# Optimization experiments

Measured on AMD Instinct MI355X. Metric: run time of the kernel, lower is better.

Reference implementation:

```python
import jax, jax.numpy as jnp
import numpy as np

HEADS = 4
DIM_HEAD = 32
DIM = 128
EPS = 1e-5


def layer_norm(x, g, b):
    m = jnp.mean(x, axis=-1, keepdims=True)
    v = jnp.var(x, axis=-1, keepdims=True)
    return (x - m) * jax.lax.rsqrt(v + EPS) * g + b


def setup_inputs() -> dict:
    key = jax.random.key(0)
    ks = jax.random.split(key, 24)
    B, D, Hb, Wb = 1, DIM, 50, 50
    N, h, w = 6, 24, 44
    Q = Hb * Wb
    NK = N * h * w
    inner = HEADS * DIM_HEAD
    s = 0.02
    inp = {
        'q': jax.random.normal(ks[0], (B, D, Hb, Wb), jnp.float32),
        'k': jax.random.normal(ks[1], (B, N, D, h, w), jnp.float32),
        'v': jax.random.normal(ks[2], (B, N, D, h, w), jnp.float32),
        'W_logits': jax.random.uniform(ks[3], (B, Q, NK), jnp.float32),
        'vis': jax.random.randint(ks[4], (B, Q, NK), 0, 2, jnp.int32),
        'skip': jax.random.normal(ks[5], (B, D, Hb, Wb), jnp.float32),
        'qn_g': jnp.ones((D,)), 'qn_b': jnp.zeros((D,)),
        'kn_g': jnp.ones((D,)), 'kn_b': jnp.zeros((D,)),
        'vn_g': jnp.ones((D,)), 'vn_b': jnp.zeros((D,)),
        'wq': s * jax.random.normal(ks[6], (inner, D)), 'bq': jnp.zeros((inner,)),
        'wk': s * jax.random.normal(ks[7], (inner, D)), 'bk': jnp.zeros((inner,)),
        'wv': s * jax.random.normal(ks[8], (inner, D)), 'bv': jnp.zeros((inner,)),
        'wproj': s * jax.random.normal(ks[9], (D, inner)), 'bproj': jnp.zeros((D,)),
        'pre_g': jnp.ones((D,)), 'pre_b': jnp.zeros((D,)),
        'w1': s * jax.random.normal(ks[10], (2 * D, D)), 'b1': jnp.zeros((2 * D,)),
        'w2': s * jax.random.normal(ks[11], (D, 2 * D)), 'b2': jnp.zeros((D,)),
        'post_g': jnp.ones((D,)), 'post_b': jnp.zeros((D,)),
    }
    return inp


def reference(q, k, v, W_logits, vis, skip,
              qn_g, qn_b, kn_g, kn_b, vn_g, vn_b,
              wq, bq, wk, bk, wv, bv, wproj, bproj,
              pre_g, pre_b, w1, b1, w2, b2, post_g, post_b):
    B, D, Hb, Wb = q.shape
    Q = Hb * Wb
    scale = DIM_HEAD ** (-0.5)
    # flatten: q -> [B, Q, D]; k,v [B,N,D,h,w] -> [B, NK, D]
    qf = q.reshape(B, D, Q).transpose(0, 2, 1)
    kf = jnp.transpose(k, (0, 1, 3, 4, 2)).reshape(B, -1, D)
    vf = jnp.transpose(v, (0, 1, 3, 4, 2)).reshape(B, -1, D)
    qf = layer_norm(qf, qn_g, qn_b) @ wq.T + bq
    kf = layer_norm(kf, kn_g, kn_b) @ wk.T + bk
    vf = layer_norm(vf, vn_g, vn_b) @ wv.T + bv
    # split heads -> [B, H, Q/K, dh]
    qh = qf.reshape(B, Q, HEADS, DIM_HEAD).transpose(0, 2, 1, 3)
    kh = kf.reshape(B, -1, HEADS, DIM_HEAD).transpose(0, 2, 1, 3)
    vh = vf.reshape(B, -1, HEADS, DIM_HEAD).transpose(0, 2, 1, 3)
    logits = jnp.einsum('bhqd,bhkd->bhqk', qh, kh) * scale
    neg_inf = jnp.finfo(logits.dtype).min
    logits = jnp.where(vis[:, None] == 0, neg_inf, logits)
    logits = logits * W_logits[:, None]
    attn = jax.nn.softmax(logits, axis=-1)
    out = jnp.einsum('bhqk,bhkd->bhqd', attn, vh)
    out = out.transpose(0, 2, 1, 3).reshape(B, Q, HEADS * DIM_HEAD)
    out = out @ wproj.T + bproj
    z = out.transpose(0, 2, 1).reshape(B, D, Hb, Wb) + skip
    zf = z.reshape(B, D, Q).transpose(0, 2, 1)
    zf = layer_norm(zf, pre_g, pre_b)
    hmid = jax.nn.gelu(zf @ w1.T + b1, approximate=False)
    zf = zf + (hmid @ w2.T + b2)
    zf = layer_norm(zf, post_g, post_b)
    return zf.transpose(0, 2, 1).reshape(B, D, Hb, Wb)
```

## Files before the change

### kernel.cpp

```cpp
#include <hip/hip_runtime.h>
#include <hip/hip_bf16.h>

typedef __attribute__((ext_vector_type(8))) short bf16x8;
typedef __attribute__((ext_vector_type(4))) float f32x4;

#define NQ 2500
#define NKK 6336
#define NHEADS 4
#define DHEAD 32
#define CSC 0.25503482f
#define BIGNEG (-1.0e30f)

#define WS_QP 0
#define WS_KP 640000
#define WS_VT 2262016
#define WS_WB 3884032
#define WS_OP 4146176
#define OSPLIT_F 340000
#define OROW_F 136
#define WS_REQ3 8226176ULL

#define WQB 0
#define WKB 16384
#define WVB 32768
#define WPROJB 49152
#define W1B 65536
#define W2B 98304

#define NTILES_TOTAL 99
#define TQ 16
#define ATQ 32
#define TK 64
#define QBLOCKS 157
#define AQBLOCKS 79

#define PSTR 72
#define ABSTR 68

__device__ __forceinline__ unsigned short bf16bits(float x) {
  union { __hip_bfloat16 h; unsigned short s; } cv;
  cv.h = __float2bfloat16(x);
  return cv.s;
}

__global__ __launch_bounds__(256) void wconv_kernel(
    const float* __restrict__ wq, const float* __restrict__ wk,
    const float* __restrict__ wv, const float* __restrict__ wproj,
    const float* __restrict__ w1, const float* __restrict__ w2,
    __hip_bfloat16* __restrict__ wb)
{
  int e = (blockIdx.x * 256 + threadIdx.x) * 4;
  const float* src; int off;
  if (e < 16384)      { src = wq;    off = e; }
  else if (e < 32768) { src = wk;    off = e - 16384; }
  else if (e < 49152) { src = wv;    off = e - 32768; }
  else if (e < 65536) { src = wproj; off = e - 49152; }
  else if (e < 98304) { src = w1;    off = e - 65536; }
  else                { src = w2;    off = e - 98304; }
  float4 v = *(const float4*)(src + off);
  ushort4 o4;
  o4.x = bf16bits(v.x); o4.y = bf16bits(v.y); o4.z = bf16bits(v.z); o4.w = bf16bits(v.w);
  *(ushort4*)((unsigned short*)wb + e) = o4;
}

__global__ __launch_bounds__(256) void lnproj_kernel(
    const float* __restrict__ qin, const float* __restrict__ kin, const float* __restrict__ vin,
    const float* __restrict__ qn_g, const float* __restrict__ qn_b,
    const float* __restrict__ kn_g, const float* __restrict__ kn_b,
    const float* __restrict__ vn_g, const float* __restrict__ vn_b,
    const __hip_bfloat16* __restrict__ wball,
    const float* __restrict__ bq, const float* __restrict__ bk, const float* __restrict__ bv,
    __hip_bfloat16* __restrict__ Qp, __hip_bfloat16* __restrict__ Kp,
    __hip_bfloat16* __restrict__ Vt)
{
  __shared__ __hip_bfloat16 lxb[32][136];
  __shared__ float lpart[32][8][2];
  __shared__ float lmr[32][2];
  __shared__ float lgb[128], lbeb[128];

  const int t = threadIdx.x;
  const int bb = blockIdx.x;
  int mode, row0;
  const float *in, *g, *be, *bo;
  const __hip_bfloat16* wb;
  if (bb < 79)       { mode = 0; row0 = bb * 32;         in = qin; g = qn_g; be = qn_b; wb = wball + WQB; bo = bq; }
  else if (bb < 277) { mode = 1; row0 = (bb - 79) * 32;  in = kin; g = kn_g; be = kn_b; wb = wball + WKB; bo = bk; }
  else               { mode = 2; row0 = (bb - 277) * 32; in = vin; g = vn_g; be = vn_b; wb = wball + WVB; bo = bv; }

  if (t < 128) { lgb[t] = g[t]; lbeb[t] = be[t]; }

  const int row = t & 31, seg = t >> 5;
  int grow = row0 + row;
  size_t base, dstr;
  bool rvalid = true;
  if (mode == 0) { rvalid = (grow < NQ); base = (size_t)(rvalid ? grow : NQ - 1); dstr = NQ; }
  else { int n = grow / 1056, rr = grow - n * 1056; base = (size_t)n * 135168 + rr; dstr = 1056; }

  float xr[16];
  float s = 0.f, ss = 0.f;
  #pragma unroll
  for (int i = 0; i < 16; ++i) {
    float x = in[base + (size_t)(seg * 16 + i) * dstr];
    xr[i] = x; s += x; ss += x * x;
  }
  lpart[row][seg][0] = s; lpart[row][seg][1] = ss;
  __syncthreads();
  if (t < 32) {
    float S = 0.f, SS = 0.f;
    #pragma unroll
    for (int j = 0; j < 8; ++j) { S += lpart[t][j][0]; SS += lpart[t][j][1]; }
    float mean = S * (1.f / 128.f);
    float var  = SS * (1.f / 128.f) - mean * mean;
    lmr[t][0] = mean;
    lmr[t][1] = rsqrtf(fmaxf(var, 0.f) + 1e-5f);
  }
  __syncthreads();
  {
    float mean = lmr[row][0], rstd = lmr[row][1];
    #pragma unroll
    for (int i = 0; i < 16; ++i) {
      int d = seg * 16 + i;
      lxb[row][d] = __float2bfloat16((xr[i] - mean) * rstd * lgb[d] + lbeb[d]);
    }
  }
  __syncthreads();

  const int wid = t >> 6, lane = t & 63;
  const int n16 = lane & 15, quad = lane >> 4;
  const int ow = wid * 32;

  f32x4 acc[2][2] = {};
  for (int kt = 0; kt < 4; ++kt) {
    bf16x8 af[2];
    #pragma unroll
    for (int mi = 0; mi < 2; ++mi)
      af[mi] = *(const bf16x8*)&lxb[mi * 16 + n16][kt * 32 + quad * 8];
    #pragma unroll
    for (int ni = 0; ni < 2; ++ni) {
      bf16x8 bw = *(const bf16x8*)(wb + (size_t)(ow + ni * 16 + n16) * 128 + kt * 32 + quad * 8);
      #pragma unroll
      for (int mi = 0; mi < 2; ++mi)
        acc[mi][ni] = __builtin_amdgcn_mfma_f32_16x16x32_bf16(af[mi], bw, acc[mi][ni], 0, 0, 0);
    }
  }

  float bias[2];
  #pragma unroll
  for (int ni = 0; ni < 2; ++ni) bias[ni] = bo[ow + ni * 16 + n16];

  #pragma unroll
  for (int mi = 0; mi < 2; ++mi) {
    int gr0 = row0 + mi * 16 + quad * 4;
    if (mode == 2) {
      #pragma unroll
      for (int ni = 0; ni < 2; ++ni) {
        int o = ow + ni * 16 + n16;
        ushort4 v4;
        v4.x = bf16bits(acc[mi][ni][0] + bias[ni]);
        v4.y = bf16bits(acc[mi][ni][1] + bias[ni]);
        v4.z = bf16bits(acc[mi][ni][2] + bias[ni]);
        v4.w = bf16bits(acc[mi][ni][3] + bias[ni]);
        *(ushort4*)((unsigned short*)Vt + (size_t)o * NKK + gr0) = v4;
      }
    } else {
      #pragma unroll
      for (int rg = 0; rg < 4; ++rg) {
        int gr = gr0 + rg;
        if (mode != 0 || gr < NQ) {
          #pragma unroll
          for (int ni = 0; ni < 2; ++ni) {
            int o = ow + ni * 16 + n16;
            __hip_bfloat16 b16 = __float2bfloat16(acc[mi][ni][rg] + bias[ni]);
            if (mode == 0) Qp[(size_t)gr * 128 + o] = b16;
            else           Kp[(size_t)gr * 128 + o] = b16;
          }
        }
      }
    }
  }
}

__global__ __launch_bounds__(256, 4) void attn_kernel(
    const __hip_bfloat16* __restrict__ Qp,
    const __hip_bfloat16* __restrict__ Kp,
    const __hip_bfloat16* __restrict__ Vt,
    const float* __restrict__ Wl,
    const int* __restrict__ vis,
    float* __restrict__ Opart)
{
  __shared__ alignas(16) float sc[2][ATQ * ABSTR];
  __shared__ alignas(16) __hip_bfloat16 lp[NHEADS * ATQ * PSTR];

  const int t = threadIdx.x;
  const int lane = t & 63;
  const int h = t >> 6;
  const int n16 = lane & 15;
  const int quad = lane >> 4;
  const int q0 = blockIdx.x * ATQ;
  const int split = blockIdx.y;
  const int ksplit = gridDim.y;
  const int tstart = (NTILES_TOTAL * split) / ksplit;
  const int ntiles = (NTILES_TOTAL * (split + 1)) / ksplit - tstart;

  bf16x8 aq[2];
  #pragma unroll
  for (int m = 0; m < 2; ++m) {
    int gqa = q0 + m * 16 + n16; if (gqa >= NQ) gqa = NQ - 1;
    aq[m] = *(const bf16x8*)(Qp + (size_t)gqa * 128 + h * DHEAD + quad * 8);
  }

  const int qq = t >> 3, kkc = (t & 7) * 8;
  int gqe = q0 + qq; if (gqe >= NQ) gqe = NQ - 1;
  const size_t wbase = (size_t)gqe * NKK + kkc;

  bf16x8 bones;
  {
    short one = (short)0x3F80;
    short val = (n16 == 0) ? one : (short)0;
    #pragma unroll
    for (int j = 0; j < 8; ++j) bones[j] = val;
  }

  float4 pw0, pw1; int4 pvs0, pvs1;

  auto issue = [&](int tile) {
    int k0 = (tstart + tile) * TK;
    pw0  = *(const float4*)(Wl + wbase + k0);
    pw1  = *(const float4*)(Wl + wbase + k0 + 4);
    pvs0 = *(const int4*)(vis + wbase + k0);
    pvs1 = *(const int4*)(vis + wbase + k0 + 4);
  };
  auto commit = [&](int buf) {
    float4 c0, c1;
    c0.x = pvs0.x ? pw0.x * CSC : BIGNEG * pw0.x;
    c0.y = pvs0.y ? pw0.y * CSC : BIGNEG * pw0.y;
    c0.z = pvs0.z ? pw0.z * CSC : BIGNEG * pw0.z;
    c0.w = pvs0.w ? pw0.w * CSC : BIGNEG * pw0.w;
    c1.x = pvs1.x ? pw1.x * CSC : BIGNEG * pw1.x;
    c1.y = pvs1.y ? pw1.y * CSC : BIGNEG * pw1.y;
    c1.z = pvs1.z ? pw1.z * CSC : BIGNEG * pw1.z;
    c1.w = pvs1.w ? pw1.w * CSC : BIGNEG * pw1.w;
    *(float4*)&sc[buf][qq * ABSTR + kkc] = c0;
    *(float4*)&sc[buf][qq * ABSTR + kkc + 4] = c1;
  };

  f32x4 o[2][3];
  #pragma unroll
  for (int m = 0; m < 2; ++m)
    #pragma unroll
    for (int j = 0; j < 3; ++j)
      o[m][j] = f32x4{0.f, 0.f, 0.f, 0.f};

  issue(0);
  commit(0);
  __syncthreads();

  for (int kt = 0; kt < ntiles; ++kt) {
    const int k0 = (tstart + kt) * TK;
    const int cur = kt & 1;
    if (kt + 1 < ntiles) issue(kt + 1);

    f32x4 s[2][4];
    #pragma unroll
    for (int ks = 0; ks < 4; ++ks) {
      bf16x8 bk = *(const bf16x8*)(Kp + (size_t)(k0 + ks * 16 + n16) * 128 + h * DHEAD + quad * 8);
      f32x4 z = {0.f, 0.f, 0.f, 0.f};
      s[0][ks] = __builtin_amdgcn_mfma_f32_16x16x32_bf16(aq[0], bk, z, 0, 0, 0);
      s[1][ks] = __builtin_amdgcn_mfma_f32_16x16x32_bf16(aq[1], bk, z, 0, 0, 0);
    }

    bf16x8 bv[2][2];
    #pragma unroll
    for (int kk = 0; kk < 2; ++kk) {
      bv[kk][0] = *(const bf16x8*)(Vt + (size_t)(h * DHEAD + n16) * NKK + k0 + kk * 32 + quad * 8);
      bv[kk][1] = *(const bf16x8*)(Vt + (size_t)(h * DHEAD + 16 + n16) * NKK + k0 + kk * 32 + quad * 8);
    }

    #pragma unroll
    for (int m = 0; m < 2; ++m) {
      #pragma unroll
      for (int ks = 0; ks < 4; ++ks) {
        #pragma unroll
        for (int r = 0; r < 4; ++r) {
          int row = m * 16 + quad * 4 + r;
          float c = sc[cur][row * ABSTR + ks * 16 + n16];
          float tt = s[m][ks][r] * c;
          float arg = (c >= 0.f) ? tt : c;
          float p = exp2f(fminf(arg, 60.f));
          lp[h * (ATQ * PSTR) + row * PSTR + ks * 16 + n16] = __float2bfloat16(p);
        }
      }
    }

    #pragma unroll
    for (int kk = 0; kk < 2; ++kk) {
      #pragma unroll
      for (int m = 0; m < 2; ++m) {
        bf16x8 ap = *(const bf16x8*)&lp[h * (ATQ * PSTR) + (m * 16 + n16) * PSTR + kk * 32 + quad * 8];
        o[m][0] = __builtin_amdgcn_mfma_f32_16x16x32_bf16(ap, bv[kk][0], o[m][0], 0, 0, 0);
        o[m][1] = __builtin_amdgcn_mfma_f32_16x16x32_bf16(ap, bv[kk][1], o[m][1], 0, 0, 0);
        o[m][2] = __builtin_amdgcn_mfma_f32_16x16x32_bf16(ap, bones, o[m][2], 0, 0, 0);
      }
    }

    if (kt + 1 < ntiles) {
      commit(cur ^ 1);
      __syncthreads();
    }
  }

  #pragma unroll
  for (int m = 0; m < 2; ++m) {
    #pragma unroll
    for (int r = 0; r < 4; ++r) {
      int gq = q0 + m * 16 + quad * 4 + r;
      if (gq < NQ) {
        float* rowp = Opart + (size_t)split * OSPLIT_F + (size_t)gq * OROW_F;
        rowp[h * DHEAD + n16] = o[m][0][r];
        rowp[h * DHEAD + 16 + n16] = o[m][1][r];
        if (n16 == 0) rowp[128 + h] = o[m][2][r];
      }
    }
  }
}

__global__ __launch_bounds__(256) void mlp_kernel(
    const float* __restrict__ Opart, int ksplit,
    const float* __restrict__ skip,
    const __hip_bfloat16* __restrict__ wball,
    const float* __restrict__ bproj,
    const float* __restrict__ pre_g, const float* __restrict__ pre_b,
    const float* __restrict__ b1, const float* __restrict__ b2,
    const float* __restrict__ post_g, const float* __restrict__ post_b,
    float* __restrict__ out)
{
  __shared__ __hip_bfloat16 sab[16][136];
  __shared__ __hip_bfloat16 znb[16][136];
  __shared__ float znf[16][132];
  __shared__ __hip_bfloat16 hb[16][264];
  __shared__ float part[16][4][2];

  const __hip_bfloat16* wprojb = wball + WPROJB;
  const __hip_bfloat16* w1b    = wball + W1B;
  const __hip_bfloat16* w2b    = wball + W2B;

  const int t = threadIdx.x;
  const int q0 = blockIdx.x * TQ;

  {
    int row = t >> 4, c0 = (t & 15) * 8;
    int gq = q0 + row; int cq = gq < NQ ? gq : NQ - 1;
    int head = c0 >> 5;
    float ll = 0.f;
    float acc8[8] = {};
    for (int s = 0; s < ksplit; ++s) {
      const float* rp = Opart + (size_t)s * OSPLIT_F + (size_t)cq * OROW_F;
      ll += rp[128 + head];
      float4 a = *(const float4*)(rp + c0);
      float4 b = *(const float4*)(rp + c0 + 4);
      acc8[0] += a.x; acc8[1] += a.y; acc8[2] += a.z; acc8[3] += a.w;
      acc8[4] += b.x; acc8[5] += b.y; acc8[6] += b.z; acc8[7] += b.w;
    }
    float rll = 1.f / fmaxf(ll, 1e-30f);
    #pragma unroll
    for (int i = 0; i < 8; ++i)
      sab[row][c0 + i] = __float2bfloat16(acc8[i] * rll);
  }
  __syncthreads();

  const int wid = t >> 6, lane = t & 63;
  const int n16 = lane & 15, quad = lane >> 4;
  const int qrow0 = q0 + quad * 4;

  f32x4 acc1[2] = {};
  for (int kt = 0; kt < 4; ++kt) {
    bf16x8 af = *(const bf16x8*)&sab[n16][kt * 32 + quad * 8];
    #pragma unroll
    for (int ni = 0; ni < 2; ++ni) {
      int o = wid * 32 + ni * 16 + n16;
      bf16x8 bw = *(const bf16x8*)(wprojb + (size_t)o * 128 + kt * 32 + quad * 8);
      acc1[ni] = __builtin_amdgcn_mfma_f32_16x16x32_bf16(af, bw, acc1[ni], 0, 0, 0);
    }
  }
  float z[2][4];
  #pragma unroll
  for (int ni = 0; ni < 2; ++ni) {
    int o = wid * 32 + ni * 16 + n16;
    float bo = bproj[o];
    if (qrow0 + 3 < NQ) {
      float4 sk = *(const float4*)(skip + (size_t)o * NQ + qrow0);
      z[ni][0] = acc1[ni][0] + bo + sk.x;
      z[ni][1] = acc1[ni][1] + bo + sk.y;
      z[ni][2] = acc1[ni][2] + bo + sk.z;
      z[ni][3] = acc1[ni][3] + bo + sk.w;
    } else {
      #pragma unroll
      for (int rg = 0; rg < 4; ++rg) {
        int cq = qrow0 + rg < NQ ? qrow0 + rg : NQ - 1;
        z[ni][rg] = acc1[ni][rg] + bo + skip[(size_t)o * NQ + cq];
      }
    }
  }
  #pragma unroll
  for (int rg = 0; rg < 4; ++rg) {
    float s = z[0][rg] + z[1][rg];
    float ss = z[0][rg] * z[0][rg] + z[1][rg] * z[1][rg];
    s += __shfl_xor(s, 1);  ss += __shfl_xor(ss, 1);
    s += __shfl_xor(s, 2);  ss += __shfl_xor(ss, 2);
    s += __shfl_xor(s, 4);  ss += __shfl_xor(ss, 4);
    s += __shfl_xor(s, 8);  ss += __shfl_xor(ss, 8);
    if (n16 == 0) { part[quad * 4 + rg][wid][0] = s; part[quad * 4 + rg][wid][1] = ss; }
  }
  __syncthreads();
  #pragma unroll
  for (int rg = 0; rg < 4; ++rg) {
    int row = quad * 4 + rg;
    float S  = part[row][0][0] + part[row][1][0] + part[row][2][0] + part[row][3][0];
    float SS = part[row][0][1] + part[row][1][1] + part[row][2][1] + part[row][3][1];
    float mean = S * (1.f / 128.f);
    float var  = SS * (1.f / 128.f) - mean * mean;
    float rstd = rsqrtf(fmaxf(var, 0.f) + 1e-5f);
    #pragma unroll
    for (int ni = 0; ni < 2; ++ni) {
      int o = wid * 32 + ni * 16 + n16;
      float zn = (z[ni][rg] - mean) * rstd * pre_g[o] + pre_b[o];
      znf[row][o] = zn;
      znb[row][o] = __float2bfloat16(zn);
    }
  }
  __syncthreads();

  f32x4 acc2[4] = {};
  for (int kt = 0; kt < 4; ++kt) {
    bf16x8 af = *(const bf16x8*)&znb[n16][kt * 32 + quad * 8];
    #pragma unroll
    for (int ni = 0; ni < 4; ++ni) {
      int j = wid * 64 + ni * 16 + n16;
      bf16x8 bw = *(const bf16x8*)(w1b + (size_t)j * 128 + kt * 32 + quad * 8);
      acc2[ni] = __builtin_amdgcn_mfma_f32_16x16x32_bf16(af, bw, acc2[ni], 0, 0, 0);
    }
  }
  #pragma unroll
  for (int ni = 0; ni < 4; ++ni) {
    int j = wid * 64 + ni * 16 + n16;
    float bj = b1[j];
    #pragma unroll
    for (int rg = 0; rg < 4; ++rg) {
      float a1 = acc2[ni][rg] + bj;
      hb[quad * 4 + rg][j] = __float2bfloat16(0.5f * a1 * (1.0f + erff(a1 * 0.70710678118654752f)));
    }
  }
  __syncthreads();

  f32x4 acc3[2] = {};
  for (int kt = 0; kt < 8; ++kt) {
    bf16x8 af = *(const bf16x8*)&hb[n16][kt * 32 + quad * 8];
    #pragma unroll
    for (int ni = 0; ni < 2; ++ni) {
      int o = wid * 32 + ni * 16 + n16;
      bf16x8 bw = *(const bf16x8*)(w2b + (size_t)o * 256 + kt * 32 + quad * 8);
      acc3[ni] = __builtin_amdgcn_mfma_f32_16x16x32_bf16(af, bw, acc3[ni], 0, 0, 0);
    }
  }
  float y[2][4];
  #pragma unroll
  for (int ni = 0; ni < 2; ++ni) {
    int o = wid * 32 + ni * 16 + n16;
    float bo = b2[o];
    #pragma unroll
    for (int rg = 0; rg < 4; ++rg)
      y[ni][rg] = znf[quad * 4 + rg][o] + acc3[ni][rg] + bo;
  }
  #pragma unroll
  for (int rg = 0; rg < 4; ++rg) {
    float s = y[0][rg] + y[1][rg];
    float ss = y[0][rg] * y[0][rg] + y[1][rg] * y[1][rg];
    s += __shfl_xor(s, 1);  ss += __shfl_xor(ss, 1);
    s += __shfl_xor(s, 2);  ss += __shfl_xor(ss, 2);
    s += __shfl_xor(s, 4);  ss += __shfl_xor(ss, 4);
    s += __shfl_xor(s, 8);  ss += __shfl_xor(ss, 8);
    if (n16 == 0) { part[quad * 4 + rg][wid][0] = s; part[quad * 4 + rg][wid][1] = ss; }
  }
  __syncthreads();
  #pragma unroll
  for (int rg = 0; rg < 4; ++rg) {
    int row = quad * 4 + rg;
    float S  = part[row][0][0] + part[row][1][0] + part[row][2][0] + part[row][3][0];
    float SS = part[row][0][1] + part[row][1][1] + part[row][2][1] + part[row][3][1];
    float mean = S * (1.f / 128.f);
    float var  = SS * (1.f / 128.f) - mean * mean;
    float rstd = rsqrtf(fmaxf(var, 0.f) + 1e-5f);
    #pragma unroll
    for (int ni = 0; ni < 2; ++ni) {
      int o = wid * 32 + ni * 16 + n16;
      y[ni][rg] = (y[ni][rg] - mean) * rstd * post_g[o] + post_b[o];
    }
  }
  #pragma unroll
  for (int ni = 0; ni < 2; ++ni) {
    int o = wid * 32 + ni * 16 + n16;
    if (qrow0 + 3 < NQ) {
      *(float4*)(out + (size_t)o * NQ + qrow0) = make_float4(y[ni][0], y[ni][1], y[ni][2], y[ni][3]);
    } else {
      #pragma unroll
      for (int rg = 0; rg < 4; ++rg)
        if (qrow0 + rg < NQ) out[(size_t)o * NQ + qrow0 + rg] = y[ni][rg];
    }
  }
}

extern "C" void kernel_launch(void* const* d_in, const int* in_sizes, int n_in,
                              void* d_out, int out_size, void* d_ws, size_t ws_size,
                              hipStream_t stream) {
  if (ws_size < WS_REQ3) return;
  int ksplit = (int)((ws_size - WS_OP) / (size_t)(OSPLIT_F * 4));
  if (ksplit > 12) ksplit = 12;
  if (ksplit < 3)  ksplit = 3;

  const float* q     = (const float*)d_in[0];
  const float* k     = (const float*)d_in[1];
  const float* v     = (const float*)d_in[2];
  const float* Wl    = (const float*)d_in[3];
  const int*   vis   = (const int*)d_in[4];
  const float* skip  = (const float*)d_in[5];
  const float* qn_g  = (const float*)d_in[6];
  const float* qn_b  = (const float*)d_in[7];
  const float* kn_g  = (const float*)d_in[8];
  const float* kn_b  = (const float*)d_in[9];
  const float* vn_g  = (const float*)d_in[10];
  const float* vn_b  = (const float*)d_in[11];
  const float* wq    = (const float*)d_in[12];
  const float* bq    = (const float*)d_in[13];
  const float* wk    = (const float*)d_in[14];
  const float* bk    = (const float*)d_in[15];
  const float* wv    = (const float*)d_in[16];
  const float* bv    = (const float*)d_in[17];
  const float* wproj = (const float*)d_in[18];
  const float* bproj = (const float*)d_in[19];
  const float* pre_g = (const float*)d_in[20];
  const float* pre_b = (const float*)d_in[21];
  const float* w1    = (const float*)d_in[22];
  const float* b1    = (const float*)d_in[23];
  const float* w2    = (const float*)d_in[24];
  const float* b2    = (const float*)d_in[25];
  const float* post_g= (const float*)d_in[26];
  const float* post_b= (const float*)d_in[27];

  char* ws = (char*)d_ws;
  __hip_bfloat16* Qp = (__hip_bfloat16*)(ws + WS_QP);
  __hip_bfloat16* Kp = (__hip_bfloat16*)(ws + WS_KP);
  __hip_bfloat16* Vt = (__hip_bfloat16*)(ws + WS_VT);
  __hip_bfloat16* Wb = (__hip_bfloat16*)(ws + WS_WB);
  float* Opart = (float*)(ws + WS_OP);

  hipLaunchKernelGGL(wconv_kernel, dim3(128), dim3(256), 0, stream,
                     wq, wk, wv, wproj, w1, w2, Wb);

  hipLaunchKernelGGL(lnproj_kernel, dim3(475), dim3(256), 0, stream,
                     q, k, v, qn_g, qn_b, kn_g, kn_b, vn_g, vn_b,
                     Wb, bq, bk, bv, Qp, Kp, Vt);

  hipLaunchKernelGGL(attn_kernel, dim3(AQBLOCKS, ksplit), dim3(256), 0, stream,
                     Qp, Kp, Vt, Wl, vis, Opart);

  hipLaunchKernelGGL(mlp_kernel, dim3(QBLOCKS), dim3(256), 0, stream,
                     Opart, ksplit, skip, Wb, bproj, pre_g, pre_b,
                     b1, b2, post_g, post_b, (float*)d_out);
}
```

Measured before the change: 248.1 us.

## Use nontemporal loads/stores in attention, flatten grid with split-major ordering, cap ksplit

The W_logits and vis streams, which are read once, now go through nontemporal loads, and the partial-output stores are nontemporal too, to reduce cache pollution. The 2D grid becomes a 1D grid in which the k-splits of one query block are adjacent, so neighbouring blocks share the same Q rows. The maximum ksplit drops from 12 to 8, which cuts the partial-sum work in the MLP kernel but gives fewer blocks to fill the GPU.

New measurement: 266.4 us. 1.07x slower.

```diff
diff --git a/kernel.cpp b/kernel.cpp
--- a/kernel.cpp
+++ b/kernel.cpp
@@ -3,6 +3,8 @@
 
 typedef __attribute__((ext_vector_type(8))) short bf16x8;
 typedef __attribute__((ext_vector_type(4))) float f32x4;
+typedef __attribute__((ext_vector_type(4))) float f4v;
+typedef __attribute__((ext_vector_type(4))) int i4v;
 
 #define NQ 2500
 #define NKK 6336
@@ -196,9 +198,10 @@
   const int h = t >> 6;
   const int n16 = lane & 15;
   const int quad = lane >> 4;
-  const int q0 = blockIdx.x * ATQ;
-  const int split = blockIdx.y;
-  const int ksplit = gridDim.y;
+  const int ksplit = gridDim.x / AQBLOCKS;
+  const int split = blockIdx.x % ksplit;
+  const int qb = blockIdx.x / ksplit;
+  const int q0 = qb * ATQ;
   const int tstart = (NTILES_TOTAL * split) / ksplit;
   const int ntiles = (NTILES_TOTAL * (split + 1)) / ksplit - tstart;
 
@@ -221,27 +224,27 @@
     for (int j = 0; j < 8; ++j) bones[j] = val;
   }
 
-  float4 pw0, pw1; int4 pvs0, pvs1;
+  f4v pw0, pw1; i4v pvs0, pvs1;
 
   auto issue = [&](int tile) {
     int k0 = (tstart + tile) * TK;
-    pw0  = *(const float4*)(Wl + wbase + k0);
-    pw1  = *(const float4*)(Wl + wbase + k0 + 4);
-    pvs0 = *(const int4*)(vis + wbase + k0);
-    pvs1 = *(const int4*)(vis + wbase + k0 + 4);
+    pw0  = __builtin_nontemporal_load((const f4v*)(Wl + wbase + k0));
+    pw1  = __builtin_nontemporal_load((const f4v*)(Wl + wbase + k0 + 4));
+    pvs0 = __builtin_nontemporal_load((const i4v*)(vis + wbase + k0));
+    pvs1 = __builtin_nontemporal_load((const i4v*)(vis + wbase + k0 + 4));
   };
   auto commit = [&](int buf) {
-    float4 c0, c1;
-    c0.x = pvs0.x ? pw0.x * CSC : BIGNEG * pw0.x;
-    c0.y = pvs0.y ? pw0.y * CSC : BIGNEG * pw0.y;
-    c0.z = pvs0.z ? pw0.z * CSC : BIGNEG * pw0.z;
-    c0.w = pvs0.w ? pw0.w * CSC : BIGNEG * pw0.w;
-    c1.x = pvs1.x ? pw1.x * CSC : BIGNEG * pw1.x;
-    c1.y = pvs1.y ? pw1.y * CSC : BIGNEG * pw1.y;
-    c1.z = pvs1.z ? pw1.z * CSC : BIGNEG * pw1.z;
-    c1.w = pvs1.w ? pw1.w * CSC : BIGNEG * pw1.w;
-    *(float4*)&sc[buf][qq * ABSTR + kkc] = c0;
-    *(float4*)&sc[buf][qq * ABSTR + kkc + 4] = c1;
+    f4v c0, c1;
+    c0[0] = pvs0[0] ? pw0[0] * CSC : BIGNEG * pw0[0];
+    c0[1] = pvs0[1] ? pw0[1] * CSC : BIGNEG * pw0[1];
+    c0[2] = pvs0[2] ? pw0[2] * CSC : BIGNEG * pw0[2];
+    c0[3] = pvs0[3] ? pw0[3] * CSC : BIGNEG * pw0[3];
+    c1[0] = pvs1[0] ? pw1[0] * CSC : BIGNEG * pw1[0];
+    c1[1] = pvs1[1] ? pw1[1] * CSC : BIGNEG * pw1[1];
+    c1[2] = pvs1[2] ? pw1[2] * CSC : BIGNEG * pw1[2];
+    c1[3] = pvs1[3] ? pw1[3] * CSC : BIGNEG * pw1[3];
+    *(f4v*)&sc[buf][qq * ABSTR + kkc] = c0;
+    *(f4v*)&sc[buf][qq * ABSTR + kkc + 4] = c1;
   };
 
   f32x4 o[2][3];
@@ -316,9 +319,9 @@
       int gq = q0 + m * 16 + quad * 4 + r;
       if (gq < NQ) {
         float* rowp = Opart + (size_t)split * OSPLIT_F + (size_t)gq * OROW_F;
-        rowp[h * DHEAD + n16] = o[m][0][r];
-        rowp[h * DHEAD + 16 + n16] = o[m][1][r];
-        if (n16 == 0) rowp[128 + h] = o[m][2][r];
+        __builtin_nontemporal_store(o[m][0][r], &rowp[h * DHEAD + n16]);
+        __builtin_nontemporal_store(o[m][1][r], &rowp[h * DHEAD + 16 + n16]);
+        if (n16 == 0) __builtin_nontemporal_store(o[m][2][r], &rowp[128 + h]);
       }
     }
   }
@@ -514,8 +517,8 @@
                               hipStream_t stream) {
   if (ws_size < WS_REQ3) return;
   int ksplit = (int)((ws_size - WS_OP) / (size_t)(OSPLIT_F * 4));
-  if (ksplit > 12) ksplit = 12;
-  if (ksplit < 3)  ksplit = 3;
+  if (ksplit > 8) ksplit = 8;
+  if (ksplit < 3) ksplit = 3;
 
   const float* q     = (const float*)d_in[0];
   const float* k     = (const float*)d_in[1];
@@ -560,7 +563,7 @@
                      q, k, v, qn_g, qn_b, kn_g, kn_b, vn_g, vn_b,
                      Wb, bq, bk, bv, Qp, Kp, Vt);
 
-  hipLaunchKernelGGL(attn_kernel, dim3(AQBLOCKS, ksplit), dim3(256), 0, stream,
+  hipLaunchKernelGGL(attn_kernel, dim3(AQBLOCKS * ksplit), dim3(256), 0, stream,
                      Qp, Kp, Vt, Wl, vis, Opart);
 
   hipLaunchKernelGGL(mlp_kernel, dim3(QBLOCKS), dim3(256), 0, stream,
```

## Halve attention query tile to 16 rows with XOR-swizzled LDS and more k-splits

Applied to the files above, without the earlier changes.

The attention kernel's query tile shrinks from 32 to 16 rows, so each wave runs a single MFMA row block. The padded LDS strides are replaced by XOR-swizzled layouts for the score-coefficient and probability buffers, and the occupancy hint rises from 4 to 5 blocks per CU. The k-split cap rises from 12 to 16 to create more parallel blocks. The trade-off is that each K/V tile loaded from global memory is now reused across half as many queries, so K/V traffic roughly doubles.

Result: slower. 291.4 us (+17.4%).

```diff
diff --git a/kernel.cpp b/kernel.cpp
--- a/kernel.cpp
+++ b/kernel.cpp
@@ -3,6 +3,8 @@
 
 typedef __attribute__((ext_vector_type(8))) short bf16x8;
 typedef __attribute__((ext_vector_type(4))) float f32x4;
+typedef __attribute__((ext_vector_type(4))) float f4v;
+typedef __attribute__((ext_vector_type(4))) int i4v;
 
 #define NQ 2500
 #define NKK 6336
@@ -29,13 +31,10 @@
 
 #define NTILES_TOTAL 99
 #define TQ 16
-#define ATQ 32
+#define ATQ 16
 #define TK 64
 #define QBLOCKS 157
-#define AQBLOCKS 79
-
-#define PSTR 72
-#define ABSTR 68
+#define AQBLOCKS 157
 
 __device__ __forceinline__ unsigned short bf16bits(float x) {
   union { __hip_bfloat16 h; unsigned short s; } cv;
@@ -180,7 +179,7 @@
   }
 }
 
-__global__ __launch_bounds__(256, 4) void attn_kernel(
+__global__ __launch_bounds__(256, 5) void attn_kernel(
     const __hip_bfloat16* __restrict__ Qp,
     const __hip_bfloat16* __restrict__ Kp,
     const __hip_bfloat16* __restrict__ Vt,
@@ -188,8 +187,8 @@
     const int* __restrict__ vis,
     float* __restrict__ Opart)
 {
-  __shared__ alignas(16) float sc[2][ATQ * ABSTR];
-  __shared__ alignas(16) __hip_bfloat16 lp[NHEADS * ATQ * PSTR];
+  __shared__ alignas(16) float sc[2][ATQ * 64];
+  __shared__ alignas(16) __hip_bfloat16 lp[NHEADS][ATQ * 64];
 
   const int t = threadIdx.x;
   const int lane = t & 63;
@@ -202,16 +201,16 @@
   const int tstart = (NTILES_TOTAL * split) / ksplit;
   const int ntiles = (NTILES_TOTAL * (split + 1)) / ksplit - tstart;
 
-  bf16x8 aq[2];
-  #pragma unroll
-  for (int m = 0; m < 2; ++m) {
-    int gqa = q0 + m * 16 + n16; if (gqa >= NQ) gqa = NQ - 1;
-    aq[m] = *(const bf16x8*)(Qp + (size_t)gqa * 128 + h * DHEAD + quad * 8);
-  }
-
-  const int qq = t >> 3, kkc = (t & 7) * 8;
+  bf16x8 aq;
+  {
+    int gqa = q0 + n16; if (gqa >= NQ) gqa = NQ - 1;
+    aq = *(const bf16x8*)(Qp + (size_t)gqa * 128 + h * DHEAD + quad * 8);
+  }
+
+  const int qq = t >> 4, kkc = (t & 15) * 4;
   int gqe = q0 + qq; if (gqe >= NQ) gqe = NQ - 1;
   const size_t wbase = (size_t)gqe * NKK + kkc;
+  const int scw = qq * 64 + (kkc ^ ((qq & 7) << 2));
 
   bf16x8 bones;
   {
@@ -221,35 +220,23 @@
     for (int j = 0; j < 8; ++j) bones[j] = val;
   }
 
-  float4 pw0, pw1; int4 pvs0, pvs1;
+  f4v pw; i4v pvs;
 
   auto issue = [&](int tile) {
     int k0 = (tstart + tile) * TK;
-    pw0  = *(const float4*)(Wl + wbase + k0);
-    pw1  = *(const float4*)(Wl + wbase + k0 + 4);
-    pvs0 = *(const int4*)(vis + wbase + k0);
-    pvs1 = *(const int4*)(vis + wbase + k0 + 4);
+    pw  = *(const f4v*)(Wl + wbase + k0);
+    pvs = *(const i4v*)(vis + wbase + k0);
   };
   auto commit = [&](int buf) {
-    float4 c0, c1;
-    c0.x = pvs0.x ? pw0.x * CSC : BIGNEG * pw0.x;
-    c0.y = pvs0.y ? pw0.y * CSC : BIGNEG * pw0.y;
-    c0.z = pvs0.z ? pw0.z * CSC : BIGNEG * pw0.z;
-    c0.w = pvs0.w ? pw0.w * CSC : BIGNEG * pw0.w;
-    c1.x = pvs1.x ? pw1.x * CSC : BIGNEG * pw1.x;
-    c1.y = pvs1.y ? pw1.y * CSC : BIGNEG * pw1.y;
-    c1.z = pvs1.z ? pw1.z * CSC : BIGNEG * pw1.z;
-    c1.w = pvs1.w ? pw1.w * CSC : BIGNEG * pw1.w;
-    *(float4*)&sc[buf][qq * ABSTR + kkc] = c0;
-    *(float4*)&sc[buf][qq * ABSTR + kkc + 4] = c1;
+    f4v c;
+    c[0] = pvs[0] ? pw[0] * CSC : BIGNEG * pw[0];
+    c[1] = pvs[1] ? pw[1] * CSC : BIGNEG * pw[1];
+    c[2] = pvs[2] ? pw[2] * CSC : BIGNEG * pw[2];
+    c[3] = pvs[3] ? pw[3] * CSC : BIGNEG * pw[3];
+    *(f4v*)&sc[buf][scw] = c;
   };
 
-  f32x4 o[2][3];
-  #pragma unroll
-  for (int m = 0; m < 2; ++m)
-    #pragma unroll
-    for (int j = 0; j < 3; ++j)
-      o[m][j] = f32x4{0.f, 0.f, 0.f, 0.f};
+  f32x4 o0 = {0.f,0.f,0.f,0.f}, o1 = {0.f,0.f,0.f,0.f}, o2 = {0.f,0.f,0.f,0.f};
 
   issue(0);
   commit(0);
@@ -260,13 +247,12 @@
     const int cur = kt & 1;
     if (kt + 1 < ntiles) issue(kt + 1);
 
-    f32x4 s[2][4];
+    f32x4 s[4];
     #pragma unroll
     for (int ks = 0; ks < 4; ++ks) {
       bf16x8 bk = *(const bf16x8*)(Kp + (size_t)(k0 + ks * 16 + n16) * 128 + h * DHEAD + quad * 8);
       f32x4 z = {0.f, 0.f, 0.f, 0.f};
-      s[0][ks] = __builtin_amdgcn_mfma_f32_16x16x32_bf16(aq[0], bk, z, 0, 0, 0);
-      s[1][ks] = __builtin_amdgcn_mfma_f32_16x16x32_bf16(aq[1], bk, z, 0, 0, 0);
+      s[ks] = __builtin_amdgcn_mfma_f32_16x16x32_bf16(aq, bk, z, 0, 0, 0);
     }
 
     bf16x8 bv[2][2];
@@ -277,30 +263,24 @@
     }
 
     #pragma unroll
-    for (int m = 0; m < 2; ++m) {
+    for (int ks = 0; ks < 4; ++ks) {
       #pragma unroll
-      for (int ks = 0; ks < 4; ++ks) {
-        #pragma unroll
-        for (int r = 0; r < 4; ++r) {
-          int row = m * 16 + quad * 4 + r;
-          float c = sc[cur][row * ABSTR + ks * 16 + n16];
-          float tt = s[m][ks][r] * c;
-          float arg = (c >= 0.f) ? tt : c;
-          float p = exp2f(fminf(arg, 60.f));
-          lp[h * (ATQ * PSTR) + row * PSTR + ks * 16 + n16] = __float2bfloat16(p);
-        }
+      for (int r = 0; r < 4; ++r) {
+        int row = quad * 4 + r;
+        float c = sc[cur][row * 64 + ((ks * 16 + n16) ^ ((row & 7) << 2))];
+        float tt = s[ks][r] * c;
+        float arg = (c >= 0.f) ? tt : c;
+        float p = exp2f(fminf(arg, 60.f));
+        lp[h][row * 64 + ((ks * 16 + n16) ^ ((row & 7) << 3))] = __float2bfloat16(p);
       }
     }
 
     #pragma unroll
     for (int kk = 0; kk < 2; ++kk) {
-      #pragma unroll
-      for (int m = 0; m < 2; ++m) {
-        bf16x8 ap = *(const bf16x8*)&lp[h * (ATQ * PSTR) + (m * 16 + n16) * PSTR + kk * 32 + quad * 8];
-        o[m][0] = __builtin_amdgcn_mfma_f32_16x16x32_bf16(ap, bv[kk][0], o[m][0], 0, 0, 0);
-        o[m][1] = __builtin_amdgcn_mfma_f32_16x16x32_bf16(ap, bv[kk][1], o[m][1], 0, 0, 0);
-        o[m][2] = __builtin_amdgcn_mfma_f32_16x16x32_bf16(ap, bones, o[m][2], 0, 0, 0);
-      }
+      bf16x8 ap = *(const bf16x8*)&lp[h][n16 * 64 + ((kk * 32 + quad * 8) ^ ((n16 & 7) << 3))];
+      o0 = __builtin_amdgcn_mfma_f32_16x16x32_bf16(ap, bv[kk][0], o0, 0, 0, 0);
+      o1 = __builtin_amdgcn_mfma_f32_16x16x32_bf16(ap, bv[kk][1], o1, 0, 0, 0);
+      o2 = __builtin_amdgcn_mfma_f32_16x16x32_bf16(ap, bones, o2, 0, 0, 0);
     }
 
     if (kt + 1 < ntiles) {
@@ -310,16 +290,13 @@
   }
 
   #pragma unroll
-  for (int m = 0; m < 2; ++m) {
-    #pragma unroll
-    for (int r = 0; r < 4; ++r) {
-      int gq = q0 + m * 16 + quad * 4 + r;
-      if (gq < NQ) {
-        float* rowp = Opart + (size_t)split * OSPLIT_F + (size_t)gq * OROW_F;
-        rowp[h * DHEAD + n16] = o[m][0][r];
-        rowp[h * DHEAD + 16 + n16] = o[m][1][r];
-        if (n16 == 0) rowp[128 + h] = o[m][2][r];
-      }
+  for (int r = 0; r < 4; ++r) {
+    int gq = q0 + quad * 4 + r;
+    if (gq < NQ) {
+      float* rowp = Opart + (size_t)split * OSPLIT_F + (size_t)gq * OROW_F;
+      rowp[h * DHEAD + n16] = o0[r];
+      rowp[h * DHEAD + 16 + n16] = o1[r];
+      if (n16 == 0) rowp[128 + h] = o2[r];
     }
   }
 }
@@ -514,7 +491,7 @@
                               hipStream_t stream) {
   if (ws_size < WS_REQ3) return;
   int ksplit = (int)((ws_size - WS_OP) / (size_t)(OSPLIT_F * 4));
-  if (ksplit > 12) ksplit = 12;
+  if (ksplit > 16) ksplit = 16;
   if (ksplit < 3)  ksplit = 3;
 
   const float* q     = (const float*)d_in[0];
```

## Double attention query tile to 64 with 512-thread blocks sharing K/V tiles

Applied to the files above, without the earlier changes.

The attention kernel now processes 64 queries per block using 8 waves (4 heads x 2 query halves), so each K/V tile fetched from global memory serves twice as many queries and the block count halves. The scale/mask tile shrinks to a single shared-memory buffer, with an extra barrier before refilling it in place of double buffering. The per-wave probability buffer is kept. The trade-off is an extra synchronisation per tile and lower occupancy (launch bounds 512,2), in exchange for fewer redundant K/V loads.

New measurement: 250.3 us. Within noise of the previous version (+0.9%).

```diff
diff --git a/kernel.cpp b/kernel.cpp
--- a/kernel.cpp
+++ b/kernel.cpp
@@ -29,10 +29,10 @@
 
 #define NTILES_TOTAL 99
 #define TQ 16
-#define ATQ 32
+#define ATQ 64
 #define TK 64
 #define QBLOCKS 157
-#define AQBLOCKS 79
+#define AQBLOCKS 40
 
 #define PSTR 72
 #define ABSTR 68
@@ -180,7 +180,7 @@
   }
 }
 
-__global__ __launch_bounds__(256, 4) void attn_kernel(
+__global__ __launch_bounds__(512, 2) void attn_kernel(
     const __hip_bfloat16* __restrict__ Qp,
     const __hip_bfloat16* __restrict__ Kp,
     const __hip_bfloat16* __restrict__ Vt,
@@ -188,12 +188,14 @@
     const int* __restrict__ vis,
     float* __restrict__ Opart)
 {
-  __shared__ alignas(16) float sc[2][ATQ * ABSTR];
-  __shared__ alignas(16) __hip_bfloat16 lp[NHEADS * ATQ * PSTR];
+  __shared__ alignas(16) float sc[ATQ * ABSTR];
+  __shared__ alignas(16) __hip_bfloat16 lp[8][32 * PSTR];
 
   const int t = threadIdx.x;
   const int lane = t & 63;
-  const int h = t >> 6;
+  const int w = t >> 6;
+  const int h = w & 3;
+  const int qh = w >> 2;
   const int n16 = lane & 15;
   const int quad = lane >> 4;
   const int q0 = blockIdx.x * ATQ;
@@ -205,7 +207,7 @@
   bf16x8 aq[2];
   #pragma unroll
   for (int m = 0; m < 2; ++m) {
-    int gqa = q0 + m * 16 + n16; if (gqa >= NQ) gqa = NQ - 1;
+    int gqa = q0 + qh * 32 + m * 16 + n16; if (gqa >= NQ) gqa = NQ - 1;
     aq[m] = *(const bf16x8*)(Qp + (size_t)gqa * 128 + h * DHEAD + quad * 8);
   }
 
@@ -230,7 +232,7 @@
     pvs0 = *(const int4*)(vis + wbase + k0);
     pvs1 = *(const int4*)(vis + wbase + k0 + 4);
   };
-  auto commit = [&](int buf) {
+  auto commit = [&]() {
     float4 c0, c1;
     c0.x = pvs0.x ? pw0.x * CSC : BIGNEG * pw0.x;
     c0.y = pvs0.y ? pw0.y * CSC : BIGNEG * pw0.y;
@@ -240,8 +242,8 @@
     c1.y = pvs1.y ? pw1.y * CSC : BIGNEG * pw1.y;
     c1.z = pvs1.z ? pw1.z * CSC : BIGNEG * pw1.z;
     c1.w = pvs1.w ? pw1.w * CSC : BIGNEG * pw1.w;
-    *(float4*)&sc[buf][qq * ABSTR + kkc] = c0;
-    *(float4*)&sc[buf][qq * ABSTR + kkc + 4] = c1;
+    *(float4*)&sc[qq * ABSTR + kkc] = c0;
+    *(float4*)&sc[qq * ABSTR + kkc + 4] = c1;
   };
 
   f32x4 o[2][3];
@@ -252,12 +254,11 @@
       o[m][j] = f32x4{0.f, 0.f, 0.f, 0.f};
 
   issue(0);
-  commit(0);
+  commit();
   __syncthreads();
 
   for (int kt = 0; kt < ntiles; ++kt) {
     const int k0 = (tstart + kt) * TK;
-    const int cur = kt & 1;
     if (kt + 1 < ntiles) issue(kt + 1);
 
     f32x4 s[2][4];
@@ -283,11 +284,11 @@
         #pragma unroll
         for (int r = 0; r < 4; ++r) {
           int row = m * 16 + quad * 4 + r;
-          float c = sc[cur][row * ABSTR + ks * 16 + n16];
+          float c = sc[(qh * 32 + row) * ABSTR + ks * 16 + n16];
           float tt = s[m][ks][r] * c;
           float arg = (c >= 0.f) ? tt : c;
           float p = exp2f(fminf(arg, 60.f));
-          lp[h * (ATQ * PSTR) + row * PSTR + ks * 16 + n16] = __float2bfloat16(p);
+          lp[w][row * PSTR + ks * 16 + n16] = __float2bfloat16(p);
         }
       }
     }
@@ -296,7 +297,7 @@
     for (int kk = 0; kk < 2; ++kk) {
       #pragma unroll
       for (int m = 0; m < 2; ++m) {
-        bf16x8 ap = *(const bf16x8*)&lp[h * (ATQ * PSTR) + (m * 16 + n16) * PSTR + kk * 32 + quad * 8];
+        bf16x8 ap = *(const bf16x8*)&lp[w][(m * 16 + n16) * PSTR + kk * 32 + quad * 8];
         o[m][0] = __builtin_amdgcn_mfma_f32_16x16x32_bf16(ap, bv[kk][0], o[m][0], 0, 0, 0);
         o[m][1] = __builtin_amdgcn_mfma_f32_16x16x32_bf16(ap, bv[kk][1], o[m][1], 0, 0, 0);
         o[m][2] = __builtin_amdgcn_mfma_f32_16x16x32_bf16(ap, bones, o[m][2], 0, 0, 0);
@@ -304,8 +305,9 @@
     }
 
     if (kt + 1 < ntiles) {
-      commit(cur ^ 1);
       __syncthreads();
+      commit();
+      __syncthreads();
     }
   }
 
@@ -313,7 +315,7 @@
   for (int m = 0; m < 2; ++m) {
     #pragma unroll
     for (int r = 0; r < 4; ++r) {
-      int gq = q0 + m * 16 + quad * 4 + r;
+      int gq = q0 + qh * 32 + m * 16 + quad * 4 + r;
       if (gq < NQ) {
         float* rowp = Opart + (size_t)split * OSPLIT_F + (size_t)gq * OROW_F;
         rowp[h * DHEAD + n16] = o[m][0][r];
@@ -560,7 +562,7 @@
                      q, k, v, qn_g, qn_b, kn_g, kn_b, vn_g, vn_b,
                      Wb, bq, bk, bv, Qp, Kp, Vt);
 
-  hipLaunchKernelGGL(attn_kernel, dim3(AQBLOCKS, ksplit), dim3(256), 0, stream,
+  hipLaunchKernelGGL(attn_kernel, dim3(AQBLOCKS, ksplit), dim3(512), 0, stream,
                      Qp, Kp, Vt, Wl, vis, Opart);
 
   hipLaunchKernelGGL(mlp_kernel, dim3(QBLOCKS), dim3(256), 0, stream,
```
